# Kernel optimization log

Hardware: AMD Instinct MI355X
Metric: run time of the kernel (lower is better)

Reference implementation:

```python
import jax, jax.numpy as jnp
import numpy as np

N, D, H, E, TOP_K = 4096, 1024, 2048, 8, 2


def setup_inputs() -> dict:
    key = jax.random.key(0)
    ks = jax.random.split(key, 8)
    s = 0.02
    return {
        "x": jax.random.normal(ks[0], (N, D), dtype=jnp.float32),
        "gate_W": jax.random.normal(ks[1], (D, E), dtype=jnp.float32) * s,
        "gate_b": jnp.zeros((E,), dtype=jnp.float32),
        "W1": jax.random.normal(ks[2], (E, D, H), dtype=jnp.float32) * s,
        "b1": jnp.zeros((E, H), dtype=jnp.float32),
        "W2": jax.random.normal(ks[3], (E, H, D), dtype=jnp.float32) * s,
        "b2": jnp.zeros((E, D), dtype=jnp.float32),
    }


def reference(x, gate_W, gate_b, W1, b1, W2, b2):
    # TopKGate: softmax over expert logits, pick top-k probs + indices.
    logits = x @ gate_W + gate_b                    # [N, E]
    probs = jax.nn.softmax(logits, axis=-1)
    gates, idxs = jax.lax.top_k(probs, TOP_K)        # [N, K] each

    # Combine weights w[n, e] = sum_k gates[n,k] * (idxs[n,k] == e).
    onehot = jax.nn.one_hot(idxs, E, dtype=x.dtype)  # [N, K, E]
    w = jnp.einsum("nke,nk->ne", onehot, gates)      # [N, E]

    # Dense per-expert MLP on all tokens; unrouted tokens get weight 0,
    # so the math matches the masked gather/scatter original exactly.
    h = jax.nn.relu(jnp.einsum("nd,edh->enh", x, W1) + b1[:, None, :])  # [E,N,H]
    y = jnp.einsum("enh,ehd->end", h, W2) + b2[:, None, :]               # [E,N,D]
    out = jnp.einsum("end,ne->nd", y, w)                                 # [N,D]
    return out
```

## Files before the change

### kernel.cpp

```cpp
#include <hip/hip_runtime.h>
#include <hip/hip_bf16.h>
#include <cstdint>

#define N_TOK 4096
#define DIM   1024
#define HID   2048
#define NE    8

typedef __bf16 bf16x8 __attribute__((ext_vector_type(8)));
typedef __bf16 bf16x4 __attribute__((ext_vector_type(4)));
typedef float  f32x4  __attribute__((ext_vector_type(4)));

__device__ __forceinline__ void gload16(const void* g, void* l) {
    __builtin_amdgcn_global_load_lds(
        (const __attribute__((address_space(1))) void*)g,
        (__attribute__((address_space(3))) void*)l, 16, 0, 0);
}

__global__ void transpose_cvt_all(const float* __restrict__ W1, const float* __restrict__ W2,
                                  __bf16* __restrict__ w1t, __bf16* __restrict__ w2t) {
    int lin = blockIdx.x;
    const float* src; __bf16* dst; int R, C, rx, cy;
    if (lin < 16384) {
        const int e = lin >> 11, rem = lin & 2047;
        rx = rem >> 6; cy = rem & 63;
        R = DIM; C = HID;
        src = W1 + (size_t)e * DIM * HID; dst = w1t + (size_t)e * DIM * HID;
    } else {
        lin -= 16384;
        const int e = lin >> 11, rem = lin & 2047;
        rx = rem >> 5; cy = rem & 31;
        R = HID; C = DIM;
        src = W2 + (size_t)e * DIM * HID; dst = w2t + (size_t)e * DIM * HID;
    }
    __shared__ float t[32][33];
    const int r0 = rx * 32, c0 = cy * 32;
    const int tr = threadIdx.x >> 3;
    const int tc = (threadIdx.x & 7) * 4;
    float4 v = *(const float4*)&src[(size_t)(r0 + tr) * C + c0 + tc];
    t[tr][tc + 0] = v.x; t[tr][tc + 1] = v.y; t[tr][tc + 2] = v.z; t[tr][tc + 3] = v.w;
    __syncthreads();
    bf16x4 o;
    o[0] = (__bf16)t[tc + 0][tr];
    o[1] = (__bf16)t[tc + 1][tr];
    o[2] = (__bf16)t[tc + 2][tr];
    o[3] = (__bf16)t[tc + 3][tr];
    *(bf16x4*)&dst[(size_t)(c0 + tr) * R + r0 + tc] = o;
}

__global__ void gate_kernel(const float* __restrict__ x, const float* __restrict__ gW,
                            const float* __restrict__ gb, int* __restrict__ top_idx,
                            float* __restrict__ top_gate, __bf16* __restrict__ xb) {
    const int tokn = blockIdx.x * 4 + (threadIdx.x >> 6);
    const int lane = threadIdx.x & 63;
    const float4* xr = (const float4*)(x + (size_t)tokn * DIM);
    __bf16* xbr = xb + (size_t)tokn * DIM;
    float acc[NE] = {};
#pragma unroll
    for (int i = 0; i < 4; i++) {
        const int v4 = i * 64 + lane;
        const float4 xv = xr[v4];
        bf16x4 xc = { (__bf16)xv.x, (__bf16)xv.y, (__bf16)xv.z, (__bf16)xv.w };
        *(bf16x4*)&xbr[v4 * 4] = xc;
        const float* wb = &gW[v4 * 4 * NE];
        const float xs[4] = { xv.x, xv.y, xv.z, xv.w };
#pragma unroll
        for (int j = 0; j < 4; j++) {
            const float4 wa = *(const float4*)&wb[j * NE];
            const float4 wc = *(const float4*)&wb[j * NE + 4];
            acc[0] += xs[j] * wa.x; acc[1] += xs[j] * wa.y;
            acc[2] += xs[j] * wa.z; acc[3] += xs[j] * wa.w;
            acc[4] += xs[j] * wc.x; acc[5] += xs[j] * wc.y;
            acc[6] += xs[j] * wc.z; acc[7] += xs[j] * wc.w;
        }
    }
#pragma unroll
    for (int e = 0; e < NE; e++)
#pragma unroll
        for (int s = 32; s > 0; s >>= 1)
            acc[e] += __shfl_down(acc[e], s, 64);
    if (lane == 0) {
        float lg[NE], p[NE];
        float mx = -1e30f;
#pragma unroll
        for (int e = 0; e < NE; e++) { lg[e] = acc[e] + gb[e]; mx = fmaxf(mx, lg[e]); }
        float s = 0.f;
#pragma unroll
        for (int e = 0; e < NE; e++) { p[e] = __expf(lg[e] - mx); s += p[e]; }
        const float inv = 1.f / s;
#pragma unroll
        for (int e = 0; e < NE; e++) p[e] *= inv;
        int i0 = 0; float p0 = p[0];
#pragma unroll
        for (int e = 1; e < NE; e++) if (p[e] > p0) { p0 = p[e]; i0 = e; }
        int i1 = -1; float p1 = -1.f;
#pragma unroll
        for (int e = 0; e < NE; e++) if (e != i0 && p[e] > p1) { p1 = p[e]; i1 = e; }
        top_idx[tokn * 2] = i0;  top_idx[tokn * 2 + 1] = i1;
        top_gate[tokn * 2] = p0; top_gate[tokn * 2 + 1] = p1;
    }
}

__global__ void count_kernel(const int* __restrict__ top_idx, int* __restrict__ cnt) {
    __shared__ int hist[NE];
    if (threadIdx.x < NE) hist[threadIdx.x] = 0;
    __syncthreads();
    const int n = blockIdx.x * 256 + threadIdx.x;
    atomicAdd(&hist[top_idx[n * 2]], 1);
    atomicAdd(&hist[top_idx[n * 2 + 1]], 1);
    __syncthreads();
    if (threadIdx.x < NE) atomicAdd(&cnt[threadIdx.x], hist[threadIdx.x]);
}

__global__ void build_kernel(const int* __restrict__ top_idx, const int* __restrict__ cnt,
                             int* __restrict__ run, int* __restrict__ row_token,
                             int* __restrict__ tok_row) {
    __shared__ int soffs[NE];
    __shared__ int lrun[NE];
    __shared__ int base[NE];
    if (threadIdx.x == 0) {
        int s = 0;
        for (int e = 0; e < NE; e++) { soffs[e] = s; s += cnt[e]; }
    }
    if (threadIdx.x < NE) lrun[threadIdx.x] = 0;
    __syncthreads();
    const int n = blockIdx.x * 256 + threadIdx.x;
    const int e0 = top_idx[n * 2], e1 = top_idx[n * 2 + 1];
    const int p0 = atomicAdd(&lrun[e0], 1);
    const int p1 = atomicAdd(&lrun[e1], 1);
    __syncthreads();
    if (threadIdx.x < NE) base[threadIdx.x] = atomicAdd(&run[threadIdx.x], lrun[threadIdx.x]);
    __syncthreads();
    const int r0 = soffs[e0] + base[e0] + p0;
    const int r1 = soffs[e1] + base[e1] + p1;
    row_token[r0] = n; tok_row[n * 2] = r0;
    row_token[r1] = n; tok_row[n * 2 + 1] = r1;
}

__global__ __launch_bounds__(256, 2) void gemm1_kernel(
    const __bf16* __restrict__ xb, const __bf16* __restrict__ w1t,
    const float* __restrict__ b1, const int* __restrict__ cnt,
    const int* __restrict__ row_token, __bf16* __restrict__ h) {
    const int lin = blockIdx.x;
    const int e   = lin & 7;
    const int t   = lin >> 3;
    const int n0  = (t & 7) * 256;
    const int mt  = t >> 3;
    int off_e = 0;
    for (int i = 0; i < e; i++) off_e += cnt[i];
    const int ce = cnt[e];
    if (mt * 128 >= ce) return;

    __shared__ __bf16 lA[8192];
    __shared__ __bf16 lB[16384];

    const int tid  = threadIdx.x;
    const int lane = tid & 63;
    const int wid  = tid >> 6;
    const int quad = lane >> 4;
    const int l16  = lane & 15;
    const int wm   = wid & 1;
    const int wn   = wid >> 1;

    const int lrow = lane >> 3;
    const int cch  = (lane & 7) ^ lrow;
    const __bf16* aros[4]; char* ldsA[4];
#pragma unroll
    for (int j = 0; j < 4; j++) {
        const int g   = wid * 4 + j;
        const int row = g * 8 + lrow;
        int gr = off_e + mt * 128 + row;
        gr = gr < 2 * N_TOK - 1 ? gr : 2 * N_TOK - 1;
        const int tok = row_token[gr] & (N_TOK - 1);
        aros[j] = xb + (size_t)tok * DIM + cch * 8;
        ldsA[j] = (char*)lA + g * 1024;
    }
    const __bf16* bros[8]; char* ldsB[8];
#pragma unroll
    for (int j = 0; j < 8; j++) {
        const int g   = wid * 8 + j;
        const int row = g * 8 + lrow;
        bros[j] = w1t + ((size_t)e * HID + n0 + row) * DIM + cch * 8;
        ldsB[j] = (char*)lB + g * 1024;
    }

    f32x4 acc[4][8] = {};

    for (int kk = 0; kk < DIM; kk += 64) {
#pragma unroll
        for (int j = 0; j < 4; j++) gload16(aros[j] + kk, ldsA[j]);
#pragma unroll
        for (int j = 0; j < 8; j++) gload16(bros[j] + kk, ldsB[j]);
        __syncthreads();
#pragma unroll
        for (int hh = 0; hh < 2; hh++) {
            const int sw = (((hh * 4 + quad) ^ (l16 & 7)) << 4);
            bf16x8 af[4], bfr[8];
#pragma unroll
            for (int mi = 0; mi < 4; mi++)
                af[mi] = *(const bf16x8*)((const char*)lA + (wm * 64 + mi * 16 + l16) * 128 + sw);
#pragma unroll
            for (int ni = 0; ni < 8; ni++)
                bfr[ni] = *(const bf16x8*)((const char*)lB + (wn * 128 + ni * 16 + l16) * 128 + sw);
#pragma unroll
            for (int mi = 0; mi < 4; mi++)
#pragma unroll
                for (int ni = 0; ni < 8; ni++)
                    acc[mi][ni] = __builtin_amdgcn_mfma_f32_16x16x32_bf16(af[mi], bfr[ni], acc[mi][ni], 0, 0, 0);
        }
        __syncthreads();
    }

#pragma unroll
    for (int ni = 0; ni < 8; ni++) {
        const int col = n0 + wn * 128 + ni * 16 + l16;
        const float bias = b1[e * HID + col];
#pragma unroll
        for (int mi = 0; mi < 4; mi++) {
#pragma unroll
            for (int r = 0; r < 4; r++) {
                const int lr = wm * 64 + mi * 16 + quad * 4 + r;
                const int gm = mt * 128 + lr;
                if (gm < ce) {
                    float v = acc[mi][ni][r] + bias;
                    v = v > 0.f ? v : 0.f;
                    h[(size_t)(off_e + gm) * HID + col] = (__bf16)v;
                }
            }
        }
    }
}

__global__ __launch_bounds__(256, 2) void gemm2_kernel(
    const __bf16* __restrict__ h, const __bf16* __restrict__ w2t,
    const float* __restrict__ b2, const int* __restrict__ cnt,
    float* __restrict__ y) {
    const int lin = blockIdx.x;
    const int e   = lin & 7;
    const int t   = lin >> 3;
    const int n0  = (t & 7) * 128;
    const int mt  = t >> 3;
    int off_e = 0;
    for (int i = 0; i < e; i++) off_e += cnt[i];
    const int ce = cnt[e];
    if (mt * 128 >= ce) return;

    __shared__ __bf16 lA[8192];
    __shared__ __bf16 lB[8192];

    const int tid  = threadIdx.x;
    const int lane = tid & 63;
    const int wid  = tid >> 6;
    const int quad = lane >> 4;
    const int l16  = lane & 15;
    const int wm   = wid & 1;
    const int wn   = wid >> 1;

    const int lrow = lane >> 3;
    const int cch  = (lane & 7) ^ lrow;
    const __bf16* aros[4]; const __bf16* bros[4];
    char* ldsA[4]; char* ldsB[4];
#pragma unroll
    for (int j = 0; j < 4; j++) {
        const int row = (wid * 4 + j) * 8 + lrow;
        int gr = off_e + mt * 128 + row;
        gr = gr < 2 * N_TOK - 1 ? gr : 2 * N_TOK - 1;
        aros[j] = h   + (size_t)gr * HID + cch * 8;
        bros[j] = w2t + ((size_t)e * DIM + n0 + row) * HID + cch * 8;
        ldsA[j] = (char*)lA + (wid * 4 + j) * 1024;
        ldsB[j] = (char*)lB + (wid * 4 + j) * 1024;
    }

    f32x4 acc[4][4] = {};

    for (int kk = 0; kk < HID; kk += 64) {
#pragma unroll
        for (int j = 0; j < 4; j++) gload16(aros[j] + kk, ldsA[j]);
#pragma unroll
        for (int j = 0; j < 4; j++) gload16(bros[j] + kk, ldsB[j]);
        __syncthreads();
#pragma unroll
        for (int hh = 0; hh < 2; hh++) {
            const int sw = (((hh * 4 + quad) ^ (l16 & 7)) << 4);
            bf16x8 af[4], bfr[4];
#pragma unroll
            for (int mi = 0; mi < 4; mi++)
                af[mi] = *(const bf16x8*)((const char*)lA + (wm * 64 + mi * 16 + l16) * 128 + sw);
#pragma unroll
            for (int ni = 0; ni < 4; ni++)
                bfr[ni] = *(const bf16x8*)((const char*)lB + (wn * 64 + ni * 16 + l16) * 128 + sw);
#pragma unroll
            for (int mi = 0; mi < 4; mi++)
#pragma unroll
                for (int ni = 0; ni < 4; ni++)
                    acc[mi][ni] = __builtin_amdgcn_mfma_f32_16x16x32_bf16(af[mi], bfr[ni], acc[mi][ni], 0, 0, 0);
        }
        __syncthreads();
    }

#pragma unroll
    for (int mi = 0; mi < 4; mi++) {
#pragma unroll
        for (int r = 0; r < 4; r++) {
            const int lr = wm * 64 + mi * 16 + quad * 4 + r;
            const int gm = mt * 128 + lr;
            if (gm < ce) {
#pragma unroll
                for (int ni = 0; ni < 4; ni++) {
                    const int col = n0 + wn * 64 + ni * 16 + l16;
                    y[(size_t)(off_e + gm) * DIM + col] = acc[mi][ni][r] + b2[e * DIM + col];
                }
            }
        }
    }
}

__global__ void combine_kernel(const float* __restrict__ y, const int* __restrict__ tok_row,
                               const float* __restrict__ top_gate, float* __restrict__ out) {
    const int n = blockIdx.x;
    const int d = threadIdx.x * 4;
    const int r0 = tok_row[n * 2], r1 = tok_row[n * 2 + 1];
    const float g0 = top_gate[n * 2], g1 = top_gate[n * 2 + 1];
    float4 a = *(const float4*)&y[(size_t)r0 * DIM + d];
    float4 b = *(const float4*)&y[(size_t)r1 * DIM + d];
    float4 o = { g0 * a.x + g1 * b.x, g0 * a.y + g1 * b.y,
                 g0 * a.z + g1 * b.z, g0 * a.w + g1 * b.w };
    *(float4*)&out[(size_t)n * DIM + d] = o;
}

extern "C" void kernel_launch(void* const* d_in, const int* in_sizes, int n_in,
                              void* d_out, int out_size, void* d_ws, size_t ws_size,
                              hipStream_t stream) {
    const float* x  = (const float*)d_in[0];
    const float* gW = (const float*)d_in[1];
    const float* gb = (const float*)d_in[2];
    const float* W1 = (const float*)d_in[3];
    const float* b1 = (const float*)d_in[4];
    const float* W2 = (const float*)d_in[5];
    const float* b2 = (const float*)d_in[6];
    float* out = (float*)d_out;

    char* ws = (char*)d_ws;
    __bf16* xb   = (__bf16*)(ws);
    __bf16* w1t  = (__bf16*)(ws + ((size_t)8  << 20));
    float*  ybuf = (float*) (ws + ((size_t)8  << 20));
    __bf16* w2t  = (__bf16*)(ws + ((size_t)40 << 20));
    __bf16* hbuf = (__bf16*)(ws + ((size_t)72 << 20));
    char* tail   = ws + ((size_t)104 << 20);
    int*   row_token = (int*)(tail);
    int*   tok_row   = (int*)(tail + 32768);
    int*   top_idx   = (int*)(tail + 65536);
    float* top_gate  = (float*)(tail + 98304);
    int*   cnt       = (int*)(tail + 131072);
    int*   run       = cnt + 32;

    hipMemsetAsync(cnt, 0, 256, stream);

    gate_kernel<<<N_TOK / 4, 256, 0, stream>>>(x, gW, gb, top_idx, top_gate, xb);
    count_kernel<<<N_TOK / 256, 256, 0, stream>>>(top_idx, cnt);
    build_kernel<<<N_TOK / 256, 256, 0, stream>>>(top_idx, cnt, run, row_token, tok_row);
    transpose_cvt_all<<<32768, 256, 0, stream>>>(W1, W2, w1t, w2t);
    gemm1_kernel<<<NE * 32 * (HID / 256), 256, 0, stream>>>(xb, w1t, b1, cnt, row_token, hbuf);
    gemm2_kernel<<<NE * 32 * (DIM / 128), 256, 0, stream>>>(hbuf, w2t, b2, cnt, ybuf);
    combine_kernel<<<N_TOK, 256, 0, stream>>>(ybuf, tok_row, top_gate, out);
}
```

Baseline: 337.9 us.

## Double-buffer LDS tiles in both expert GEMMs and shrink gemm1 N tile

Both grouped GEMM kernels now use two LDS buffers per operand. The next K-slice is prefetched via global_load_lds right after a single barrier, so global loads overlap the MFMA work on the current slice and the trailing barrier is dropped. gemm1's output tile also shrinks from 128x256 to 128x128, which cuts accumulator registers and doubles the grid. The costs are more LDS per block (64KB), which may limit occupancy, and less B-tile reuse in gemm1.

```diff
diff --git a/kernel.cpp b/kernel.cpp
--- a/kernel.cpp
+++ b/kernel.cpp
@@ -144,15 +144,15 @@
     const int lin = blockIdx.x;
     const int e   = lin & 7;
     const int t   = lin >> 3;
-    const int n0  = (t & 7) * 256;
-    const int mt  = t >> 3;
+    const int n0  = (t & 15) * 128;
+    const int mt  = t >> 4;
     int off_e = 0;
     for (int i = 0; i < e; i++) off_e += cnt[i];
     const int ce = cnt[e];
     if (mt * 128 >= ce) return;
 
-    __shared__ __bf16 lA[8192];
-    __shared__ __bf16 lB[16384];
+    __shared__ __bf16 lA[2][8192];
+    __shared__ __bf16 lB[2][8192];
 
     const int tid  = threadIdx.x;
     const int lane = tid & 63;
@@ -164,7 +164,8 @@
 
     const int lrow = lane >> 3;
     const int cch  = (lane & 7) ^ lrow;
-    const __bf16* aros[4]; char* ldsA[4];
+    const __bf16* aros[4]; const __bf16* bros[4];
+    int ldsoff[4];
 #pragma unroll
     for (int j = 0; j < 4; j++) {
         const int g   = wid * 4 + j;
@@ -172,48 +173,49 @@
         int gr = off_e + mt * 128 + row;
         gr = gr < 2 * N_TOK - 1 ? gr : 2 * N_TOK - 1;
         const int tok = row_token[gr] & (N_TOK - 1);
-        aros[j] = xb + (size_t)tok * DIM + cch * 8;
-        ldsA[j] = (char*)lA + g * 1024;
-    }
-    const __bf16* bros[8]; char* ldsB[8];
-#pragma unroll
-    for (int j = 0; j < 8; j++) {
-        const int g   = wid * 8 + j;
-        const int row = g * 8 + lrow;
+        aros[j] = xb  + (size_t)tok * DIM + cch * 8;
         bros[j] = w1t + ((size_t)e * HID + n0 + row) * DIM + cch * 8;
-        ldsB[j] = (char*)lB + g * 1024;
-    }
-
-    f32x4 acc[4][8] = {};
+        ldsoff[j] = g * 1024;
+    }
+
+    f32x4 acc[4][4] = {};
+
+#pragma unroll
+    for (int j = 0; j < 4; j++) gload16(aros[j], (char*)lA[0] + ldsoff[j]);
+#pragma unroll
+    for (int j = 0; j < 4; j++) gload16(bros[j], (char*)lB[0] + ldsoff[j]);
 
     for (int kk = 0; kk < DIM; kk += 64) {
-#pragma unroll
-        for (int j = 0; j < 4; j++) gload16(aros[j] + kk, ldsA[j]);
-#pragma unroll
-        for (int j = 0; j < 8; j++) gload16(bros[j] + kk, ldsB[j]);
+        const int b = (kk >> 6) & 1;
         __syncthreads();
+        if (kk + 64 < DIM) {
+            const int nb = b ^ 1;
+#pragma unroll
+            for (int j = 0; j < 4; j++) gload16(aros[j] + kk + 64, (char*)lA[nb] + ldsoff[j]);
+#pragma unroll
+            for (int j = 0; j < 4; j++) gload16(bros[j] + kk + 64, (char*)lB[nb] + ldsoff[j]);
+        }
 #pragma unroll
         for (int hh = 0; hh < 2; hh++) {
             const int sw = (((hh * 4 + quad) ^ (l16 & 7)) << 4);
-            bf16x8 af[4], bfr[8];
+            bf16x8 af[4], bfr[4];
 #pragma unroll
             for (int mi = 0; mi < 4; mi++)
-                af[mi] = *(const bf16x8*)((const char*)lA + (wm * 64 + mi * 16 + l16) * 128 + sw);
-#pragma unroll
-            for (int ni = 0; ni < 8; ni++)
-                bfr[ni] = *(const bf16x8*)((const char*)lB + (wn * 128 + ni * 16 + l16) * 128 + sw);
+                af[mi] = *(const bf16x8*)((const char*)lA[b] + (wm * 64 + mi * 16 + l16) * 128 + sw);
+#pragma unroll
+            for (int ni = 0; ni < 4; ni++)
+                bfr[ni] = *(const bf16x8*)((const char*)lB[b] + (wn * 64 + ni * 16 + l16) * 128 + sw);
 #pragma unroll
             for (int mi = 0; mi < 4; mi++)
 #pragma unroll
-                for (int ni = 0; ni < 8; ni++)
+                for (int ni = 0; ni < 4; ni++)
                     acc[mi][ni] = __builtin_amdgcn_mfma_f32_16x16x32_bf16(af[mi], bfr[ni], acc[mi][ni], 0, 0, 0);
         }
-        __syncthreads();
-    }
-
-#pragma unroll
-    for (int ni = 0; ni < 8; ni++) {
-        const int col = n0 + wn * 128 + ni * 16 + l16;
+    }
+
+#pragma unroll
+    for (int ni = 0; ni < 4; ni++) {
+        const int col = n0 + wn * 64 + ni * 16 + l16;
         const float bias = b1[e * HID + col];
 #pragma unroll
         for (int mi = 0; mi < 4; mi++) {
@@ -245,8 +247,8 @@
     const int ce = cnt[e];
     if (mt * 128 >= ce) return;
 
-    __shared__ __bf16 lA[8192];
-    __shared__ __bf16 lB[8192];
+    __shared__ __bf16 lA[2][8192];
+    __shared__ __bf16 lB[2][8192];
 
     const int tid  = threadIdx.x;
     const int lane = tid & 63;
@@ -259,43 +261,51 @@
     const int lrow = lane >> 3;
     const int cch  = (lane & 7) ^ lrow;
     const __bf16* aros[4]; const __bf16* bros[4];
-    char* ldsA[4]; char* ldsB[4];
+    int ldsoff[4];
 #pragma unroll
     for (int j = 0; j < 4; j++) {
-        const int row = (wid * 4 + j) * 8 + lrow;
+        const int g   = wid * 4 + j;
+        const int row = g * 8 + lrow;
         int gr = off_e + mt * 128 + row;
         gr = gr < 2 * N_TOK - 1 ? gr : 2 * N_TOK - 1;
         aros[j] = h   + (size_t)gr * HID + cch * 8;
         bros[j] = w2t + ((size_t)e * DIM + n0 + row) * HID + cch * 8;
-        ldsA[j] = (char*)lA + (wid * 4 + j) * 1024;
-        ldsB[j] = (char*)lB + (wid * 4 + j) * 1024;
+        ldsoff[j] = g * 1024;
     }
 
     f32x4 acc[4][4] = {};
 
+#pragma unroll
+    for (int j = 0; j < 4; j++) gload16(aros[j], (char*)lA[0] + ldsoff[j]);
+#pragma unroll
+    for (int j = 0; j < 4; j++) gload16(bros[j], (char*)lB[0] + ldsoff[j]);
+
     for (int kk = 0; kk < HID; kk += 64) {
-#pragma unroll
-        for (int j = 0; j < 4; j++) gload16(aros[j] + kk, ldsA[j]);
-#pragma unroll
-        for (int j = 0; j < 4; j++) gload16(bros[j] + kk, ldsB[j]);
+        const int b = (kk >> 6) & 1;
         __syncthreads();
+        if (kk + 64 < HID) {
+            const int nb = b ^ 1;
+#pragma unroll
+            for (int j = 0; j < 4; j++) gload16(aros[j] + kk + 64, (char*)lA[nb] + ldsoff[j]);
+#pragma unroll
+            for (int j = 0; j < 4; j++) gload16(bros[j] + kk + 64, (char*)lB[nb] + ldsoff[j]);
+        }
 #pragma unroll
         for (int hh = 0; hh < 2; hh++) {
             const int sw = (((hh * 4 + quad) ^ (l16 & 7)) << 4);
             bf16x8 af[4], bfr[4];
 #pragma unroll
             for (int mi = 0; mi < 4; mi++)
-                af[mi] = *(const bf16x8*)((const char*)lA + (wm * 64 + mi * 16 + l16) * 128 + sw);
+                af[mi] = *(const bf16x8*)((const char*)lA[b] + (wm * 64 + mi * 16 + l16) * 128 + sw);
 #pragma unroll
             for (int ni = 0; ni < 4; ni++)
-                bfr[ni] = *(const bf16x8*)((const char*)lB + (wn * 64 + ni * 16 + l16) * 128 + sw);
+                bfr[ni] = *(const bf16x8*)((const char*)lB[b] + (wn * 64 + ni * 16 + l16) * 128 + sw);
 #pragma unroll
             for (int mi = 0; mi < 4; mi++)
 #pragma unroll
                 for (int ni = 0; ni < 4; ni++)
                     acc[mi][ni] = __builtin_amdgcn_mfma_f32_16x16x32_bf16(af[mi], bfr[ni], acc[mi][ni], 0, 0, 0);
         }
-        __syncthreads();
     }
 
 #pragma unroll
@@ -360,7 +370,7 @@
     count_kernel<<<N_TOK / 256, 256, 0, stream>>>(top_idx, cnt);
     build_kernel<<<N_TOK / 256, 256, 0, stream>>>(top_idx, cnt, run, row_token, tok_row);
     transpose_cvt_all<<<32768, 256, 0, stream>>>(W1, W2, w1t, w2t);
-    gemm1_kernel<<<NE * 32 * (HID / 256), 256, 0, stream>>>(xb, w1t, b1, cnt, row_token, hbuf);
+    gemm1_kernel<<<NE * 32 * (HID / 128), 256, 0, stream>>>(xb, w1t, b1, cnt, row_token, hbuf);
     gemm2_kernel<<<NE * 32 * (DIM / 128), 256, 0, stream>>>(hbuf, w2t, b2, cnt, ybuf);
     combine_kernel<<<N_TOK, 256, 0, stream>>>(ybuf, tok_row, top_gate, out);
 }
```

Measured after the change: 360.7 us. 1.07x slower.
